# Kernel optimization log

Measured on AMD Instinct MI355X. Metric: run time of the kernel, lower is better.

Reference implementation:

```python
import jax, jax.numpy as jnp
import numpy as np

B, QLEN, MLEN, D_MODEL, N_HEAD, D_HEAD = 4, 1024, 1024, 512, 8, 64
KLEN = QLEN + MLEN


def _rel_shift(x):
    # x: [b, i, j, n] -> Transformer-XL relative shift
    b, i, j, n = x.shape
    zero_pad = jnp.zeros((b, i, 1, n), dtype=x.dtype)
    x_padded = jnp.concatenate([zero_pad, x], axis=2)          # [b, i, j+1, n]
    x_padded = x_padded.reshape(b, j + 1, i, n)
    return x_padded[:, 1:].reshape(b, i, j, n)


def setup_inputs() -> dict:
    key = jax.random.key(0)
    ks = jax.random.split(key, 9)
    x = jax.random.normal(ks[0], (B, KLEN, D_MODEL), dtype=jnp.float32)
    p = jax.random.normal(ks[1], (KLEN, D_MODEL), dtype=jnp.float32)
    w_scale = 0.02
    W_query = jax.random.normal(ks[2], (D_MODEL, N_HEAD, D_HEAD), dtype=jnp.float32) * w_scale
    W_key = jax.random.normal(ks[3], (D_MODEL, N_HEAD, D_HEAD), dtype=jnp.float32) * w_scale
    W_value = jax.random.normal(ks[4], (D_MODEL, N_HEAD, D_HEAD), dtype=jnp.float32) * w_scale
    W_out = jax.random.normal(ks[5], (D_MODEL, N_HEAD, D_HEAD), dtype=jnp.float32) * w_scale
    W_position = jax.random.normal(ks[6], (D_MODEL, N_HEAD, D_HEAD), dtype=jnp.float32) * w_scale
    bias_k = jax.random.normal(ks[7], (N_HEAD, D_HEAD), dtype=jnp.float32) * w_scale
    bias_r = jax.random.normal(ks[8], (N_HEAD, D_HEAD), dtype=jnp.float32) * w_scale
    # causal mask with memory: query i attends to keys j <= i + MLEN
    i_idx = jnp.arange(QLEN)[:, None]
    j_idx = jnp.arange(KLEN)[None, :]
    mask = j_idx > (i_idx + MLEN)  # True = masked out
    return {
        "x": x, "p": p,
        "W_query": W_query, "W_key": W_key, "W_value": W_value,
        "W_out": W_out, "W_position": W_position,
        "bias_k": bias_k, "bias_r": bias_r,
        "mask": mask, "qlen": QLEN,
    }


def reference(x, p, W_query, W_key, W_value, W_out, W_position, bias_k, bias_r, mask, qlen):
    d_head = W_query.shape[-1]
    scale = 1.0 / (d_head ** 0.5)
    q = jnp.einsum('dha,bld->blha', W_query, x[:, -qlen:])   # [b, qlen, n, d]
    k = jnp.einsum('dha,bld->blha', W_key, x)                # [b, klen, n, d]
    v = jnp.einsum('dha,bld->blha', W_value, x)              # [b, klen, n, d]
    r = jnp.einsum('dha,ld->lha', W_position, p)             # [klen, n, d]
    AC = jnp.einsum('bind,bjnd->bijn', q + bias_k, k)
    BD = jnp.einsum('bind,jnd->bijn', q + bias_r, r)
    attn_score = scale * (AC + _rel_shift(BD))               # [b, i, j, n]
    neg_inf = jnp.finfo(attn_score.dtype).min
    attn_score = jnp.where(mask[None, :, :, None], neg_inf, attn_score)
    attn_prob = jax.nn.softmax(attn_score, axis=2)
    out = jnp.einsum('bijn,bjnd->bind', attn_prob, v)        # [b, qlen, n, d]
    out = jnp.einsum('dha,blha->bld', W_out, out)            # [b, qlen, d_model]
    return out
```

## Files before the change

kernel.cpp:

```cpp
#include <hip/hip_runtime.h>
#include <hip/hip_bf16.h>
#include <stddef.h>
#include <stdint.h>

#define DM    512
#define NHEAD 8
#define DHEAD 64
#define QLEN  1024
#define KLEN  2048
#define MLEN  1024
#define B_SZ  4

typedef __attribute__((ext_vector_type(8))) short short8;
typedef __attribute__((ext_vector_type(8))) unsigned short ushort8;
typedef __attribute__((ext_vector_type(4))) float floatx4;

static __device__ __forceinline__ unsigned short f2bf(float f) {
  unsigned int u = __float_as_uint(f);
  unsigned int r = (u + 0x7FFFu + ((u >> 16) & 1u)) >> 16;
  return (unsigned short)r;
}
static __device__ __forceinline__ float bf2f(unsigned short h) {
  return __uint_as_float(((unsigned int)h) << 16);
}

template <int CTRL>
static __device__ __forceinline__ float maxdpp(float v) {
  int sh = __builtin_amdgcn_update_dpp(0, __float_as_int(v), CTRL, 0xF, 0xF, true);
  return fmaxf(v, __int_as_float(sh));
}
static __device__ __forceinline__ float rowmax16(float v) {
  v = maxdpp<0xB1>(v);
  v = maxdpp<0x4E>(v);
  v = maxdpp<0x124>(v);
  v = maxdpp<0x128>(v);
  return v;
}

#define GLOAD_LDS16(gsrc, ldst)                                               \
  __builtin_amdgcn_global_load_lds(                                           \
      (const __attribute__((address_space(1))) unsigned int*)(gsrc),          \
      (__attribute__((address_space(3))) unsigned int*)(ldst), 16, 0, 0)

__global__ __launch_bounds__(256) void k_prep(
    const float* __restrict__ x, const float* __restrict__ p,
    const float* __restrict__ Wq, const float* __restrict__ Wk,
    const float* __restrict__ Wv, const float* __restrict__ Wp,
    const float* __restrict__ Wo,
    unsigned short* __restrict__ xb, unsigned short* __restrict__ pb,
    unsigned short* __restrict__ wt,
    unsigned short* __restrict__ woh, unsigned short* __restrict__ wol) {
  __shared__ float tile[64][65];
  const int bid = blockIdx.x;
  const int tid = threadIdx.x;
  if (bid < 2048) {
    const int i = bid * 256 + tid;
    float4 a = *(const float4*)(x + (size_t)i * 8);
    float4 b = *(const float4*)(x + (size_t)i * 8 + 4);
    ushort8 o;
    o[0] = f2bf(a.x); o[1] = f2bf(a.y); o[2] = f2bf(a.z); o[3] = f2bf(a.w);
    o[4] = f2bf(b.x); o[5] = f2bf(b.y); o[6] = f2bf(b.z); o[7] = f2bf(b.w);
    *(ushort8*)(xb + (size_t)i * 8) = o;
  } else if (bid < 2560) {
    const int i = (bid - 2048) * 256 + tid;
    float4 a = *(const float4*)(p + (size_t)i * 8);
    float4 b = *(const float4*)(p + (size_t)i * 8 + 4);
    ushort8 o;
    o[0] = f2bf(a.x); o[1] = f2bf(a.y); o[2] = f2bf(a.z); o[3] = f2bf(a.w);
    o[4] = f2bf(b.x); o[5] = f2bf(b.y); o[6] = f2bf(b.z); o[7] = f2bf(b.w);
    *(ushort8*)(pb + (size_t)i * 8) = o;
  } else if (bid < 2816) {
    const int b2 = bid - 2560;
    const int nbq = b2 & 7, kbq = (b2 >> 3) & 7, z = b2 >> 6;
    const float* W = (z == 0) ? Wq : (z == 1) ? Wk : (z == 2) ? Wv : Wp;
    unsigned short* out = wt + (size_t)z * 262144;
    const int row = tid >> 2, c0 = (tid & 3) * 16;
    const int kb = kbq * 64, nb = nbq * 64;
#pragma unroll
    for (int j = 0; j < 4; ++j) {
      float4 ld = *(const float4*)(W + (size_t)(kb + row) * DM + nb + c0 + j * 4);
      tile[row][c0 + j * 4 + 0] = ld.x;
      tile[row][c0 + j * 4 + 1] = ld.y;
      tile[row][c0 + j * 4 + 2] = ld.z;
      tile[row][c0 + j * 4 + 3] = ld.w;
    }
    __syncthreads();
    unsigned short ob[16];
#pragma unroll
    for (int j = 0; j < 16; ++j) ob[j] = f2bf(tile[c0 + j][row]);
    unsigned short* orow = out + (size_t)(nb + row) * DM + kb + c0;
    *(ushort8*)(orow) = *(ushort8*)&ob[0];
    *(ushort8*)(orow + 8) = *(ushort8*)&ob[8];
  } else {
    const int i = (bid - 2816) * 256 + tid;
    ushort8 vh, vl;
#pragma unroll
    for (int j = 0; j < 8; ++j) {
      float f = Wo[(size_t)i * 8 + j];
      unsigned short h = f2bf(f);
      vh[j] = h;
      vl[j] = f2bf(f - bf2f(h));
    }
    *(ushort8*)(woh + (size_t)i * 8) = vh;
    *(ushort8*)(wol + (size_t)i * 8) = vl;
  }
}

__global__ __launch_bounds__(256) void k_vtrans(
    const unsigned short* __restrict__ v_, unsigned short* __restrict__ vt) {
  __shared__ unsigned short tile[64][72];
  const int tid = threadIdx.x;
  const int row = tid >> 2, c0 = (tid & 3) * 16;
  const int kt = blockIdx.x;
  const int bn = blockIdx.y;
  const int bb = bn >> 3, n = bn & 7;
  const unsigned short* src =
      v_ + ((size_t)(bb * KLEN) + kt * 64 + row) * DM + n * DHEAD + c0;
  *(ushort8*)&tile[row][c0] = *(const ushort8*)src;
  *(ushort8*)&tile[row][c0 + 8] = *(const ushort8*)(src + 8);
  __syncthreads();
  unsigned short ob[16];
#pragma unroll
  for (int j = 0; j < 16; ++j) ob[j] = tile[c0 + j][row];
  unsigned short* dst =
      vt + ((size_t)bn * DHEAD + row) * KLEN + kt * 64 + c0;
  *(ushort8*)dst = *(ushort8*)&ob[0];
  *(ushort8*)(dst + 8) = *(ushort8*)&ob[8];
}

__global__ __launch_bounds__(256) void k_proj_mfma(
    const unsigned short* __restrict__ xb, const unsigned short* __restrict__ pb,
    const unsigned short* __restrict__ wt,
    unsigned short* __restrict__ q_, unsigned short* __restrict__ k_,
    unsigned short* __restrict__ v_, unsigned short* __restrict__ r_) {
  __shared__ unsigned short Abuf[128 * 64];
  __shared__ unsigned short Bbuf[128 * 64];
  const int tid = threadIdx.x, w = tid >> 6, lane = tid & 63;
  const int c = lane & 15, g = lane >> 4;
  const int wr = w >> 1, wc = w & 1;
  const int mb = blockIdx.x, nb = blockIdx.y;
  int prob, mloc;
  const unsigned short* A;
  unsigned short* C;
  if (mb < 32)        { prob = 0; mloc = mb;       A = xb; C = q_; }
  else if (mb < 96)   { prob = 1; mloc = mb - 32;  A = xb; C = k_; }
  else if (mb < 160)  { prob = 2; mloc = mb - 96;  A = xb; C = v_; }
  else                { prob = 3; mloc = mb - 160; A = pb; C = r_; }
  const unsigned short* W = wt + (size_t)prob * 262144;
  const int m0 = mloc * 128;
  const int lrow = lane >> 3, lslot = lane & 7;

  floatx4 acc[4][4];
#pragma unroll
  for (int m = 0; m < 4; ++m)
#pragma unroll
    for (int nn = 0; nn < 4; ++nn) acc[m][nn] = (floatx4){0.f, 0.f, 0.f, 0.f};

  for (int k0 = 0; k0 < DM; k0 += 64) {
    __syncthreads();
#pragma unroll
    for (int iq = 0; iq < 4; ++iq) {
      const int r0 = w * 32 + iq * 8;
      const int arow = r0 + lrow;
      const int mrow = m0 + arow;
      const int grow =
          (prob == 0) ? ((mrow >> 10) * KLEN + (mrow & 1023) + MLEN) : mrow;
      const int sgA = lslot ^ (arow & 7);
      GLOAD_LDS16(A + (size_t)grow * DM + k0 + sgA * 8, Abuf + r0 * 64);
      const int nrow = nb * 128 + arow;
      GLOAD_LDS16(W + (size_t)nrow * DM + k0 + sgA * 8, Bbuf + r0 * 64);
    }
    __syncthreads();
#pragma unroll
    for (int kk = 0; kk < 2; ++kk) {
      short8 af[4], bf[4];
#pragma unroll
      for (int m = 0; m < 4; ++m) {
        const int arow = wr * 64 + m * 16 + c;
        const int slot = (kk * 4 + g) ^ (arow & 7);
        af[m] = *(const short8*)(Abuf + arow * 64 + slot * 8);
      }
#pragma unroll
      for (int nn = 0; nn < 4; ++nn) {
        const int brow = wc * 64 + nn * 16 + c;
        const int slot = (kk * 4 + g) ^ (brow & 7);
        bf[nn] = *(const short8*)(Bbuf + brow * 64 + slot * 8);
      }
#pragma unroll
      for (int m = 0; m < 4; ++m)
#pragma unroll
        for (int nn = 0; nn < 4; ++nn)
          acc[m][nn] = __builtin_amdgcn_mfma_f32_16x16x32_bf16(
              af[m], bf[nn], acc[m][nn], 0, 0, 0);
    }
  }
#pragma unroll
  for (int m = 0; m < 4; ++m)
#pragma unroll
    for (int nn = 0; nn < 4; ++nn)
#pragma unroll
      for (int rg = 0; rg < 4; ++rg) {
        const int row = m0 + wr * 64 + m * 16 + 4 * g + rg;
        const int col = nb * 128 + wc * 64 + nn * 16 + c;
        C[(size_t)row * DM + col] = f2bf(acc[m][nn][rg]);
      }
}

__global__ __launch_bounds__(256) void k_out_mfma(
    const unsigned short* __restrict__ Ah, const unsigned short* __restrict__ Al,
    const unsigned short* __restrict__ Bh, const unsigned short* __restrict__ Bl,
    float* __restrict__ C) {
  __shared__ unsigned short bufAh[64 * 64], bufAl[64 * 64];
  __shared__ unsigned short bufBh[64 * 64], bufBl[64 * 64];
  const int tid = threadIdx.x, w = tid >> 6, lane = tid & 63;
  const int c = lane & 15, g = lane >> 4;
  const int wr = w >> 1, wc = w & 1;
  const int bm = blockIdx.x, bn = blockIdx.y;
  const int lrow = lane >> 3, lslot = lane & 7;
  floatx4 acc[2][2];
#pragma unroll
  for (int mi = 0; mi < 2; ++mi)
#pragma unroll
    for (int ni = 0; ni < 2; ++ni) acc[mi][ni] = (floatx4){0.f, 0.f, 0.f, 0.f};

  for (int k0 = 0; k0 < DM; k0 += 64) {
    __syncthreads();
#pragma unroll
    for (int iq = 0; iq < 2; ++iq) {
      const int r0 = w * 16 + iq * 8;
      const int arow = r0 + lrow;
      const int sg = lslot ^ (arow & 7);
      GLOAD_LDS16(Ah + (size_t)(bm * 64 + arow) * DM + k0 + sg * 8, bufAh + r0 * 64);
      GLOAD_LDS16(Al + (size_t)(bm * 64 + arow) * DM + k0 + sg * 8, bufAl + r0 * 64);
      GLOAD_LDS16(Bh + (size_t)(bn * 64 + arow) * DM + k0 + sg * 8, bufBh + r0 * 64);
      GLOAD_LDS16(Bl + (size_t)(bn * 64 + arow) * DM + k0 + sg * 8, bufBl + r0 * 64);
    }
    __syncthreads();
#pragma unroll
    for (int kk = 0; kk < 2; ++kk) {
      short8 ah[2], al[2], bh[2], bl[2];
#pragma unroll
      for (int mi = 0; mi < 2; ++mi) {
        const int row = wr * 32 + mi * 16 + c;
        const int slot = (kk * 4 + g) ^ (row & 7);
        ah[mi] = *(const short8*)(bufAh + row * 64 + slot * 8);
        al[mi] = *(const short8*)(bufAl + row * 64 + slot * 8);
      }
#pragma unroll
      for (int ni = 0; ni < 2; ++ni) {
        const int row = wc * 32 + ni * 16 + c;
        const int slot = (kk * 4 + g) ^ (row & 7);
        bh[ni] = *(const short8*)(bufBh + row * 64 + slot * 8);
        bl[ni] = *(const short8*)(bufBl + row * 64 + slot * 8);
      }
#pragma unroll
      for (int mi = 0; mi < 2; ++mi)
#pragma unroll
        for (int ni = 0; ni < 2; ++ni) {
          acc[mi][ni] = __builtin_amdgcn_mfma_f32_16x16x32_bf16(
              ah[mi], bh[ni], acc[mi][ni], 0, 0, 0);
          acc[mi][ni] = __builtin_amdgcn_mfma_f32_16x16x32_bf16(
              al[mi], bh[ni], acc[mi][ni], 0, 0, 0);
          acc[mi][ni] = __builtin_amdgcn_mfma_f32_16x16x32_bf16(
              ah[mi], bl[ni], acc[mi][ni], 0, 0, 0);
        }
    }
  }
#pragma unroll
  for (int mi = 0; mi < 2; ++mi)
#pragma unroll
    for (int ni = 0; ni < 2; ++ni)
#pragma unroll
      for (int rg = 0; rg < 4; ++rg) {
        const int row = bm * 64 + wr * 32 + mi * 16 + 4 * g + rg;
        const int col = bn * 64 + wc * 32 + ni * 16 + c;
        C[(size_t)row * DM + col] = acc[mi][ni][rg];
      }
}

__global__ __launch_bounds__(256, 2) void k_attn_mfma(
    const unsigned short* __restrict__ q, const unsigned short* __restrict__ k,
    const unsigned short* __restrict__ vt, const unsigned short* __restrict__ r,
    const float* __restrict__ bk, const float* __restrict__ br,
    unsigned short* __restrict__ aoh, unsigned short* __restrict__ aol) {
  __shared__ unsigned short Kt[2][64 * 64];
  __shared__ unsigned short VTt[2][64 * 64];
  __shared__ unsigned short Rr[192 * 64];
  __shared__ unsigned short P[4][16][76];

  const int tid = threadIdx.x;
  const int w = tid >> 6;
  const int lane = tid & 63;
  const int c = lane & 15;
  const int g = lane >> 4;
  const int n = blockIdx.y;
  const int b = blockIdx.z;
  const int grp = (n + NHEAD * b) >> 4;
  const int i0 = (grp ? (15 - (int)blockIdx.x) : (int)blockIdx.x) * 64;
  const int qb = i0 + w * 16;

  const unsigned short* vtbn = vt + (size_t)(b * NHEAD + n) * DHEAD * KLEN;
  const unsigned short* kbase = k + (size_t)(b * KLEN) * DM + n * DHEAD;
  const unsigned short* rbase_p = r + n * DHEAD;

  const int srow = tid >> 3;
  const int sslot = tid & 7;
  const int gbase = 960 - i0;

  short8 aqk[2], aqr[2];
  {
    const unsigned short* qrow =
        q + ((size_t)(b * QLEN) + qb + c) * DM + n * DHEAD;
#pragma unroll
    for (int kb2 = 0; kb2 < 2; ++kb2) {
      short8 qv = *(const short8*)(qrow + kb2 * 32 + g * 8);
#pragma unroll
      for (int j = 0; j < 8; ++j) {
        int d = kb2 * 32 + g * 8 + j;
        float f = bf2f((unsigned short)qv[j]);
        aqk[kb2][j] = (short)f2bf((f + bk[n * DHEAD + d]) * 0.125f);
        aqr[kb2][j] = (short)f2bf((f + br[n * DHEAD + d]) * 0.125f);
      }
    }
  }

  floatx4 o[4];
#pragma unroll
  for (int t = 0; t < 4; ++t) o[t] = (floatx4){0.f, 0.f, 0.f, 0.f};
  float m[4], lsum[4], shc[4];
#pragma unroll
  for (int rg = 0; rg < 4; ++rg) { m[rg] = -1e30f; lsum[rg] = 0.f; shc[rg] = 0.f; }

  const int nkb = i0 / 64 + 17;

  auto STAGE_KV = [&](int t, int buf) {
    const int j0 = t * 64;
#pragma unroll
    for (int p = 0; p < 2; ++p) {
      const int row = p * 32 + srow;
      const int sg = sslot ^ (row & 7);
      GLOAD_LDS16(kbase + (size_t)(j0 + row) * DM + sg * 8,
                  &Kt[buf][row * 64 + sslot * 8]);
      GLOAD_LDS16(vtbn + (size_t)row * KLEN + j0 + sg * 8,
                  &VTt[buf][row * 64 + sslot * 8]);
    }
  };
  auto STAGE_R = [&](int t, int bt) {
    int sb = bt + 128; if (sb >= 192) sb -= 192;
#pragma unroll
    for (int p = 0; p < 2; ++p) {
      const int row = p * 32 + srow;
      const int slot = sb + row;
      const int grow = min(gbase + 64 * t + 128 + row, KLEN - 1);
      const int sg = sslot ^ (slot & 7);
      GLOAD_LDS16(rbase_p + (size_t)grow * DM + sg * 8,
                  &Rr[slot * 64 + sslot * 8]);
    }
  };

  STAGE_KV(0, 0);
#pragma unroll
  for (int p = 0; p < 4; ++p) {
    const int row = p * 32 + srow;
    const int grow = min(gbase + row, KLEN - 1);
    const int sg = sslot ^ (row & 7);
    GLOAD_LDS16(rbase_p + (size_t)grow * DM + sg * 8,
                &Rr[row * 64 + sslot * 8]);
  }
  __syncthreads();
  int cur = 0;
  int bt = 0;

  const int s0 = (g ^ (c & 7)) * 8;
  const int s1 = ((4 + g) ^ (c & 7)) * 8;

  for (int t = 0; t < nkb; ++t) {
    if (t + 1 < nkb) { STAGE_KV(t + 1, cur ^ 1); STAGE_R(t, bt); }
    const unsigned short* Kc = &Kt[cur][0];
    const unsigned short* Vc = &VTt[cur][0];

    float sh[5][4];
    if (t == 0) {
      const int lr = (3 - w) * 16 + c;
      const unsigned short* Rrow = Rr + lr * 64;
      short8 rf0 = *(const short8*)(Rrow + s0);
      short8 rf1 = *(const short8*)(Rrow + s1);
      floatx4 bd = (floatx4){0.f, 0.f, 0.f, 0.f};
      bd = __builtin_amdgcn_mfma_f32_16x16x32_bf16(aqr[0], rf0, bd, 0, 0, 0);
      bd = __builtin_amdgcn_mfma_f32_16x16x32_bf16(aqr[1], rf1, bd, 0, 0, 0);
#pragma unroll
      for (int rg = 0; rg < 4; ++rg) {
        const int srcl = (g << 4) | ((15 + c - 4 * g - rg) & 15);
        sh[0][rg] = __shfl(bd[rg], srcl, 64);
      }
    } else {
#pragma unroll
      for (int rg = 0; rg < 4; ++rg) sh[0][rg] = shc[rg];
    }
#pragma unroll
    for (int tau5 = 1; tau5 < 5; ++tau5) {
      const int lr = (tau5 + 3 - w) * 16 + c;
      int slot = bt + lr; if (slot >= 192) slot -= 192;
      const unsigned short* Rrow = Rr + slot * 64;
      short8 rf0 = *(const short8*)(Rrow + s0);
      short8 rf1 = *(const short8*)(Rrow + s1);
      floatx4 bd = (floatx4){0.f, 0.f, 0.f, 0.f};
      bd = __builtin_amdgcn_mfma_f32_16x16x32_bf16(aqr[0], rf0, bd, 0, 0, 0);
      bd = __builtin_amdgcn_mfma_f32_16x16x32_bf16(aqr[1], rf1, bd, 0, 0, 0);
#pragma unroll
      for (int rg = 0; rg < 4; ++rg) {
        const int srcl = (g << 4) | ((15 + c - 4 * g - rg) & 15);
        sh[tau5][rg] = __shfl(bd[rg], srcl, 64);
      }
    }
#pragma unroll
    for (int rg = 0; rg < 4; ++rg) shc[rg] = sh[4][rg];

    floatx4 s[4];
    const bool lastblk = (t == nkb - 1);
    __builtin_amdgcn_s_setprio(1);
#pragma unroll
    for (int tau = 0; tau < 4; ++tau) {
      const int kr = tau * 16 + c;
      short8 kf0 = *(const short8*)(Kc + kr * 64 + s0);
      short8 kf1 = *(const short8*)(Kc + kr * 64 + s1);
      floatx4 acc = (floatx4){0.f, 0.f, 0.f, 0.f};
      acc = __builtin_amdgcn_mfma_f32_16x16x32_bf16(aqk[0], kf0, acc, 0, 0, 0);
      acc = __builtin_amdgcn_mfma_f32_16x16x32_bf16(aqk[1], kf1, acc, 0, 0, 0);
#pragma unroll
      for (int rg = 0; rg < 4; ++rg) {
        const int ql = 4 * g + rg;
        float sv = acc[rg] + ((c > ql) ? sh[tau + 1][rg] : sh[tau][rg]);
        if (lastblk && (tau * 16 + c > w * 16 + ql)) sv = -1e30f;
        s[tau][rg] = sv;
      }
    }
    __builtin_amdgcn_s_setprio(0);

    float mx[4];
    bool ok = true;
#pragma unroll
    for (int rg = 0; rg < 4; ++rg) {
      float v2 = fmaxf(fmaxf(s[0][rg], s[1][rg]), fmaxf(s[2][rg], s[3][rg]));
      v2 = rowmax16(v2);
      mx[rg] = v2;
      ok = ok && (v2 <= m[rg] + 8.0f);
    }
    if (!__all(ok)) {
#pragma unroll
      for (int rg = 0; rg < 4; ++rg) {
        float mn = fmaxf(m[rg], mx[rg]);
        float fac = __expf(m[rg] - mn);
        m[rg] = mn;
        lsum[rg] *= fac;
#pragma unroll
        for (int td = 0; td < 4; ++td) o[td][rg] *= fac;
      }
    }
#pragma unroll
    for (int tau = 0; tau < 4; ++tau) {
#pragma unroll
      for (int rg = 0; rg < 4; ++rg) {
        float p = __expf(s[tau][rg] - m[rg]);
        lsum[rg] += p;
        P[w][4 * g + rg][tau * 16 + c] = f2bf(p);
      }
    }

    short8 pa0 = *(const short8*)&P[w][c][g * 8];
    short8 pa1 = *(const short8*)&P[w][c][32 + g * 8];
    __builtin_amdgcn_s_setprio(1);
#pragma unroll
    for (int td = 0; td < 4; ++td) {
      const int vrow = td * 16 + c;
      short8 vb0 = *(const short8*)(Vc + vrow * 64 + s0);
      short8 vb1 = *(const short8*)(Vc + vrow * 64 + s1);
      o[td] = __builtin_amdgcn_mfma_f32_16x16x32_bf16(pa0, vb0, o[td], 0, 0, 0);
      o[td] = __builtin_amdgcn_mfma_f32_16x16x32_bf16(pa1, vb1, o[td], 0, 0, 0);
    }
    __builtin_amdgcn_s_setprio(0);
    __syncthreads();
    cur ^= 1;
    bt += 64; if (bt >= 192) bt -= 192;
  }

#pragma unroll
  for (int rg = 0; rg < 4; ++rg) {
    float L = lsum[rg];
#pragma unroll
    for (int shm = 1; shm < 16; shm <<= 1) L += __shfl_xor(L, shm, 64);
    lsum[rg] = L;
  }
#pragma unroll
  for (int rg = 0; rg < 4; ++rg) {
    const int ql = 4 * g + rg;
    const float invl = 1.0f / lsum[rg];
#pragma unroll
    for (int td = 0; td < 4; ++td) {
      float val = o[td][rg] * invl;
      unsigned short hi = f2bf(val);
      float lo = val - bf2f(hi);
      size_t off = ((size_t)(b * QLEN) + qb + ql) * DM + n * DHEAD + td * 16 + c;
      aoh[off] = hi;
      aol[off] = f2bf(lo);
    }
  }
}

extern "C" void kernel_launch(void* const* d_in, const int* in_sizes, int n_in,
                              void* d_out, int out_size, void* d_ws, size_t ws_size,
                              hipStream_t stream) {
  const float* x  = (const float*)d_in[0];
  const float* p  = (const float*)d_in[1];
  const float* Wq = (const float*)d_in[2];
  const float* Wk = (const float*)d_in[3];
  const float* Wv = (const float*)d_in[4];
  const float* Wo = (const float*)d_in[5];
  const float* Wp = (const float*)d_in[6];
  const float* bk = (const float*)d_in[7];
  const float* br = (const float*)d_in[8];
  float* out = (float*)d_out;

  unsigned short* q_  = (unsigned short*)d_ws;
  unsigned short* k_  = q_  + (size_t)2097152;
  unsigned short* v_  = k_  + (size_t)4194304;
  unsigned short* r_  = v_  + (size_t)4194304;
  unsigned short* xb  = r_  + (size_t)1048576;
  unsigned short* pb  = xb  + (size_t)4194304;
  unsigned short* wt  = pb  + (size_t)1048576;
  unsigned short* woh = wt  + (size_t)1048576;
  unsigned short* wol = woh + (size_t)262144;
  unsigned short* aoh = wol + (size_t)262144;
  unsigned short* aol = aoh + (size_t)2097152;
  unsigned short* vt_ = aol + (size_t)2097152;

  k_prep<<<2944, 256, 0, stream>>>(x, p, Wq, Wk, Wv, Wp, Wo,
                                   xb, pb, wt, woh, wol);
  k_proj_mfma<<<dim3(176, 4), 256, 0, stream>>>(xb, pb, wt, q_, k_, v_, r_);
  k_vtrans<<<dim3(KLEN / 64, NHEAD * B_SZ), 256, 0, stream>>>(v_, vt_);
  k_attn_mfma<<<dim3(16, 8, 4), 256, 0, stream>>>(
      q_, k_, vt_, r_, bk, br, aoh, aol);
  k_out_mfma<<<dim3(64, 8), 256, 0, stream>>>(aoh, aol, woh, wol, out);
}
```

Before: 115.6 us.

## Split attention key range across two wave groups with LDS merge

The attention kernel now launches 512 threads per block. Two groups of four waves each process half of the key range, using 32-wide key tiles instead of 64-wide. Group 1 writes its partial output, max and sum to shared memory, and group 0 merges them with a flash-decoding-style rescale before the final store. The aim is to double the waves per block, hide latency better, and shorten the per-block serial loop. In exchange it adds a combine step, an extra barrier and larger shared memory use, which may limit occupancy.

```diff
diff --git a/kernel.cpp b/kernel.cpp
--- a/kernel.cpp
+++ b/kernel.cpp
@@ -278,18 +278,23 @@
       }
 }
 
-__global__ __launch_bounds__(256, 2) void k_attn_mfma(
+__global__ __launch_bounds__(512, 4) void k_attn_mfma(
     const unsigned short* __restrict__ q, const unsigned short* __restrict__ k,
     const unsigned short* __restrict__ vt, const unsigned short* __restrict__ r,
     const float* __restrict__ bk, const float* __restrict__ br,
     unsigned short* __restrict__ aoh, unsigned short* __restrict__ aol) {
-  __shared__ unsigned short Kt[2][64 * 64];
-  __shared__ unsigned short VTt[2][64 * 64];
-  __shared__ unsigned short Rr[192 * 64];
-  __shared__ unsigned short P[4][16][76];
+  __shared__ alignas(16) char SMEM[75776];
+  unsigned short* Kt  = (unsigned short*)SMEM;
+  unsigned short* VTt = (unsigned short*)(SMEM + 16384);
+  unsigned short* Rr  = (unsigned short*)(SMEM + 32768);
+  unsigned short* P   = (unsigned short*)(SMEM + 65536);
+  float* oC  = (float*)SMEM;
+  float* mlC = (float*)(SMEM + 17408);
 
   const int tid = threadIdx.x;
-  const int w = tid >> 6;
+  const int wave = tid >> 6;
+  const int h = wave >> 2;
+  const int w = wave & 3;
   const int lane = tid & 63;
   const int c = lane & 15;
   const int g = lane >> 4;
@@ -303,9 +308,9 @@
   const unsigned short* kbase = k + (size_t)(b * KLEN) * DM + n * DHEAD;
   const unsigned short* rbase_p = r + n * DHEAD;
 
-  const int srow = tid >> 3;
-  const int sslot = tid & 7;
-  const int gbase = 960 - i0;
+  const int nkb = i0 / 32 + 34;
+  const int nIt = nkb >> 1;
+  const int g0r = 960 - i0;
 
   short8 aqk[2], aqr[2];
   {
@@ -331,157 +336,174 @@
 #pragma unroll
   for (int rg = 0; rg < 4; ++rg) { m[rg] = -1e30f; lsum[rg] = 0.f; shc[rg] = 0.f; }
 
-  const int nkb = i0 / 64 + 17;
-
-  auto STAGE_KV = [&](int t, int buf) {
-    const int j0 = t * 64;
-#pragma unroll
-    for (int p = 0; p < 2; ++p) {
-      const int row = p * 32 + srow;
-      const int sg = sslot ^ (row & 7);
-      GLOAD_LDS16(kbase + (size_t)(j0 + row) * DM + sg * 8,
-                  &Kt[buf][row * 64 + sslot * 8]);
-      GLOAD_LDS16(vtbn + (size_t)row * KLEN + j0 + sg * 8,
-                  &VTt[buf][row * 64 + sslot * 8]);
+  int bt = 0;
+
+  auto STAGE = [&](int itn) {
+    const int buf = itn & 1;
+    const int hh = tid >> 8;
+    const int idx = tid & 255;
+    const int tn = hh * nIt + itn;
+    {
+      const int row = idx >> 3, slot = idx & 7;
+      GLOAD_LDS16(kbase + (size_t)(32 * tn + row) * DM + (slot ^ (row & 7)) * 8,
+                  Kt + (hh * 2 + buf) * 2048 + idx * 8);
+    }
+    {
+      const int row = idx >> 2, slot = idx & 3;
+      GLOAD_LDS16(vtbn + (size_t)row * KLEN + 32 * tn +
+                      ((slot ^ ((row >> 1) & 3)) * 8),
+                  VTt + (hh * 2 + buf) * 2048 + idx * 8);
+    }
+    {
+      const int row = idx >> 3, slot = idx & 7;
+      const int sb = (bt + 96) & 127;
+      const int gst = g0r + hh * (32 * nIt);
+      const int grow = min(gst + 32 * itn + 64 + row, KLEN - 1);
+      GLOAD_LDS16(rbase_p + (size_t)grow * DM + (slot ^ (row & 7)) * 8,
+                  Rr + hh * 8192 + (sb + row) * 64 + slot * 8);
     }
   };
-  auto STAGE_R = [&](int t, int bt) {
-    int sb = bt + 128; if (sb >= 192) sb -= 192;
-#pragma unroll
-    for (int p = 0; p < 2; ++p) {
-      const int row = p * 32 + srow;
-      const int slot = sb + row;
-      const int grow = min(gbase + 64 * t + 128 + row, KLEN - 1);
-      const int sg = sslot ^ (slot & 7);
-      GLOAD_LDS16(rbase_p + (size_t)grow * DM + sg * 8,
-                  &Rr[slot * 64 + sslot * 8]);
-    }
-  };
-
-  STAGE_KV(0, 0);
-#pragma unroll
-  for (int p = 0; p < 4; ++p) {
-    const int row = p * 32 + srow;
-    const int grow = min(gbase + row, KLEN - 1);
-    const int sg = sslot ^ (row & 7);
-    GLOAD_LDS16(rbase_p + (size_t)grow * DM + sg * 8,
-                &Rr[row * 64 + sslot * 8]);
+
+  {
+    const int hh = tid >> 8;
+    const int idx = tid & 255;
+    const int tn = hh * nIt;
+    {
+      const int row = idx >> 3, slot = idx & 7;
+      GLOAD_LDS16(kbase + (size_t)(32 * tn + row) * DM + (slot ^ (row & 7)) * 8,
+                  Kt + (hh * 2) * 2048 + idx * 8);
+    }
+    {
+      const int row = idx >> 2, slot = idx & 3;
+      GLOAD_LDS16(vtbn + (size_t)row * KLEN + 32 * tn +
+                      ((slot ^ ((row >> 1) & 3)) * 8),
+                  VTt + (hh * 2) * 2048 + idx * 8);
+    }
+  }
+#pragma unroll
+  for (int p = 0; p < 3; ++p) {
+    const int Lr = tid + p * 512;
+    const int hh = (Lr >= 768) ? 1 : 0;
+    const int idx = Lr - hh * 768;
+    const int row = idx >> 3, slot = idx & 7;
+    const int gst = g0r + hh * (32 * nIt);
+    const int grow = min(gst + row, KLEN - 1);
+    GLOAD_LDS16(rbase_p + (size_t)grow * DM + (slot ^ (row & 7)) * 8,
+                Rr + hh * 8192 + row * 64 + slot * 8);
   }
   __syncthreads();
-  int cur = 0;
-  int bt = 0;
 
   const int s0 = (g ^ (c & 7)) * 8;
   const int s1 = ((4 + g) ^ (c & 7)) * 8;
-
-  for (int t = 0; t < nkb; ++t) {
-    if (t + 1 < nkb) { STAGE_KV(t + 1, cur ^ 1); STAGE_R(t, bt); }
-    const unsigned short* Kc = &Kt[cur][0];
-    const unsigned short* Vc = &VTt[cur][0];
-
-    float sh[5][4];
-    if (t == 0) {
-      const int lr = (3 - w) * 16 + c;
-      const unsigned short* Rrow = Rr + lr * 64;
-      short8 rf0 = *(const short8*)(Rrow + s0);
-      short8 rf1 = *(const short8*)(Rrow + s1);
-      floatx4 bd = (floatx4){0.f, 0.f, 0.f, 0.f};
-      bd = __builtin_amdgcn_mfma_f32_16x16x32_bf16(aqr[0], rf0, bd, 0, 0, 0);
-      bd = __builtin_amdgcn_mfma_f32_16x16x32_bf16(aqr[1], rf1, bd, 0, 0, 0);
+  const int vs0 = (g ^ ((c >> 1) & 3)) * 8;
+  unsigned short* Pw = P + (size_t)wave * 640;
+
+  for (int it = 0; it < nIt; ++it) {
+    if (it + 1 < nIt) STAGE(it + 1);
+    const int t = h * nIt + it;
+    const bool act = (32 * t <= qb + 15 + MLEN);
+    if (act) {
+      const unsigned short* Kc = Kt + (h * 2 + (it & 1)) * 2048;
+      const unsigned short* Vc = VTt + (h * 2 + (it & 1)) * 2048;
+      const unsigned short* Rh = Rr + h * 8192;
+
+      float sh[3][4];
+      if (it == 0) {
+        const int rs = ((bt + 16 * (3 - w)) & 127) + c;
+        const unsigned short* Rrow = Rh + rs * 64;
+        short8 rf0 = *(const short8*)(Rrow + s0);
+        short8 rf1 = *(const short8*)(Rrow + s1);
+        floatx4 bd = (floatx4){0.f, 0.f, 0.f, 0.f};
+        bd = __builtin_amdgcn_mfma_f32_16x16x32_bf16(aqr[0], rf0, bd, 0, 0, 0);
+        bd = __builtin_amdgcn_mfma_f32_16x16x32_bf16(aqr[1], rf1, bd, 0, 0, 0);
+#pragma unroll
+        for (int rg = 0; rg < 4; ++rg) {
+          const int srcl = (g << 4) | ((15 + c - 4 * g - rg) & 15);
+          sh[0][rg] = __shfl(bd[rg], srcl, 64);
+        }
+      } else {
+#pragma unroll
+        for (int rg = 0; rg < 4; ++rg) sh[0][rg] = shc[rg];
+      }
+#pragma unroll
+      for (int t5 = 1; t5 < 3; ++t5) {
+        const int rs = ((bt + 16 * (t5 + 3 - w)) & 127) + c;
+        const unsigned short* Rrow = Rh + rs * 64;
+        short8 rf0 = *(const short8*)(Rrow + s0);
+        short8 rf1 = *(const short8*)(Rrow + s1);
+        floatx4 bd = (floatx4){0.f, 0.f, 0.f, 0.f};
+        bd = __builtin_amdgcn_mfma_f32_16x16x32_bf16(aqr[0], rf0, bd, 0, 0, 0);
+        bd = __builtin_amdgcn_mfma_f32_16x16x32_bf16(aqr[1], rf1, bd, 0, 0, 0);
+#pragma unroll
+        for (int rg = 0; rg < 4; ++rg) {
+          const int srcl = (g << 4) | ((15 + c - 4 * g - rg) & 15);
+          sh[t5][rg] = __shfl(bd[rg], srcl, 64);
+        }
+      }
+#pragma unroll
+      for (int rg = 0; rg < 4; ++rg) shc[rg] = sh[2][rg];
+
+      const int thr = qb + MLEN - 32 * t;
+      floatx4 s[2];
+      __builtin_amdgcn_s_setprio(1);
+#pragma unroll
+      for (int tau = 0; tau < 2; ++tau) {
+        const int kr = tau * 16 + c;
+        short8 kf0 = *(const short8*)(Kc + kr * 64 + s0);
+        short8 kf1 = *(const short8*)(Kc + kr * 64 + s1);
+        floatx4 acc = (floatx4){0.f, 0.f, 0.f, 0.f};
+        acc = __builtin_amdgcn_mfma_f32_16x16x32_bf16(aqk[0], kf0, acc, 0, 0, 0);
+        acc = __builtin_amdgcn_mfma_f32_16x16x32_bf16(aqk[1], kf1, acc, 0, 0, 0);
+#pragma unroll
+        for (int rg = 0; rg < 4; ++rg) {
+          const int ql = 4 * g + rg;
+          float sv = acc[rg] + ((c > ql) ? sh[tau + 1][rg] : sh[tau][rg]);
+          if (tau * 16 + c > thr + ql) sv = -1e30f;
+          s[tau][rg] = sv;
+        }
+      }
+      __builtin_amdgcn_s_setprio(0);
+
+      float mx[4];
+      bool ok = true;
 #pragma unroll
       for (int rg = 0; rg < 4; ++rg) {
-        const int srcl = (g << 4) | ((15 + c - 4 * g - rg) & 15);
-        sh[0][rg] = __shfl(bd[rg], srcl, 64);
-      }
-    } else {
-#pragma unroll
-      for (int rg = 0; rg < 4; ++rg) sh[0][rg] = shc[rg];
-    }
-#pragma unroll
-    for (int tau5 = 1; tau5 < 5; ++tau5) {
-      const int lr = (tau5 + 3 - w) * 16 + c;
-      int slot = bt + lr; if (slot >= 192) slot -= 192;
-      const unsigned short* Rrow = Rr + slot * 64;
-      short8 rf0 = *(const short8*)(Rrow + s0);
-      short8 rf1 = *(const short8*)(Rrow + s1);
-      floatx4 bd = (floatx4){0.f, 0.f, 0.f, 0.f};
-      bd = __builtin_amdgcn_mfma_f32_16x16x32_bf16(aqr[0], rf0, bd, 0, 0, 0);
-      bd = __builtin_amdgcn_mfma_f32_16x16x32_bf16(aqr[1], rf1, bd, 0, 0, 0);
-#pragma unroll
-      for (int rg = 0; rg < 4; ++rg) {
-        const int srcl = (g << 4) | ((15 + c - 4 * g - rg) & 15);
-        sh[tau5][rg] = __shfl(bd[rg], srcl, 64);
-      }
-    }
-#pragma unroll
-    for (int rg = 0; rg < 4; ++rg) shc[rg] = sh[4][rg];
-
-    floatx4 s[4];
-    const bool lastblk = (t == nkb - 1);
-    __builtin_amdgcn_s_setprio(1);
-#pragma unroll
-    for (int tau = 0; tau < 4; ++tau) {
-      const int kr = tau * 16 + c;
-      short8 kf0 = *(const short8*)(Kc + kr * 64 + s0);
-      short8 kf1 = *(const short8*)(Kc + kr * 64 + s1);
-      floatx4 acc = (floatx4){0.f, 0.f, 0.f, 0.f};
-      acc = __builtin_amdgcn_mfma_f32_16x16x32_bf16(aqk[0], kf0, acc, 0, 0, 0);
-      acc = __builtin_amdgcn_mfma_f32_16x16x32_bf16(aqk[1], kf1, acc, 0, 0, 0);
-#pragma unroll
-      for (int rg = 0; rg < 4; ++rg) {
-        const int ql = 4 * g + rg;
-        float sv = acc[rg] + ((c > ql) ? sh[tau + 1][rg] : sh[tau][rg]);
-        if (lastblk && (tau * 16 + c > w * 16 + ql)) sv = -1e30f;
-        s[tau][rg] = sv;
-      }
-    }
-    __builtin_amdgcn_s_setprio(0);
-
-    float mx[4];
-    bool ok = true;
-#pragma unroll
-    for (int rg = 0; rg < 4; ++rg) {
-      float v2 = fmaxf(fmaxf(s[0][rg], s[1][rg]), fmaxf(s[2][rg], s[3][rg]));
-      v2 = rowmax16(v2);
-      mx[rg] = v2;
-      ok = ok && (v2 <= m[rg] + 8.0f);
-    }
-    if (!__all(ok)) {
-#pragma unroll
-      for (int rg = 0; rg < 4; ++rg) {
-        float mn = fmaxf(m[rg], mx[rg]);
-        float fac = __expf(m[rg] - mn);
-        m[rg] = mn;
-        lsum[rg] *= fac;
-#pragma unroll
-        for (int td = 0; td < 4; ++td) o[td][rg] *= fac;
-      }
-    }
-#pragma unroll
-    for (int tau = 0; tau < 4; ++tau) {
-#pragma unroll
-      for (int rg = 0; rg < 4; ++rg) {
-        float p = __expf(s[tau][rg] - m[rg]);
-        lsum[rg] += p;
-        P[w][4 * g + rg][tau * 16 + c] = f2bf(p);
-      }
-    }
-
-    short8 pa0 = *(const short8*)&P[w][c][g * 8];
-    short8 pa1 = *(const short8*)&P[w][c][32 + g * 8];
-    __builtin_amdgcn_s_setprio(1);
-#pragma unroll
-    for (int td = 0; td < 4; ++td) {
-      const int vrow = td * 16 + c;
-      short8 vb0 = *(const short8*)(Vc + vrow * 64 + s0);
-      short8 vb1 = *(const short8*)(Vc + vrow * 64 + s1);
-      o[td] = __builtin_amdgcn_mfma_f32_16x16x32_bf16(pa0, vb0, o[td], 0, 0, 0);
-      o[td] = __builtin_amdgcn_mfma_f32_16x16x32_bf16(pa1, vb1, o[td], 0, 0, 0);
-    }
-    __builtin_amdgcn_s_setprio(0);
+        float v2 = rowmax16(fmaxf(s[0][rg], s[1][rg]));
+        mx[rg] = v2;
+        ok = ok && (v2 <= m[rg] + 8.0f);
+      }
+      if (!__all(ok)) {
+#pragma unroll
+        for (int rg = 0; rg < 4; ++rg) {
+          float mn = fmaxf(m[rg], mx[rg]);
+          float fac = __expf(m[rg] - mn);
+          m[rg] = mn;
+          lsum[rg] *= fac;
+#pragma unroll
+          for (int td = 0; td < 4; ++td) o[td][rg] *= fac;
+        }
+      }
+#pragma unroll
+      for (int tau = 0; tau < 2; ++tau) {
+#pragma unroll
+        for (int rg = 0; rg < 4; ++rg) {
+          float p = __expf(s[tau][rg] - m[rg]);
+          lsum[rg] += p;
+          Pw[(4 * g + rg) * 40 + tau * 16 + c] = f2bf(p);
+        }
+      }
+
+      short8 pa = *(const short8*)(Pw + c * 40 + g * 8);
+      __builtin_amdgcn_s_setprio(1);
+#pragma unroll
+      for (int td = 0; td < 4; ++td) {
+        short8 vb = *(const short8*)(Vc + (td * 16 + c) * 32 + vs0);
+        o[td] = __builtin_amdgcn_mfma_f32_16x16x32_bf16(pa, vb, o[td], 0, 0, 0);
+      }
+      __builtin_amdgcn_s_setprio(0);
+    }
     __syncthreads();
-    cur ^= 1;
-    bt += 64; if (bt >= 192) bt -= 192;
+    bt = (bt + 32) & 127;
   }
 
 #pragma unroll
@@ -491,18 +513,40 @@
     for (int shm = 1; shm < 16; shm <<= 1) L += __shfl_xor(L, shm, 64);
     lsum[rg] = L;
   }
-#pragma unroll
-  for (int rg = 0; rg < 4; ++rg) {
-    const int ql = 4 * g + rg;
-    const float invl = 1.0f / lsum[rg];
-#pragma unroll
-    for (int td = 0; td < 4; ++td) {
-      float val = o[td][rg] * invl;
-      unsigned short hi = f2bf(val);
-      float lo = val - bf2f(hi);
-      size_t off = ((size_t)(b * QLEN) + qb + ql) * DM + n * DHEAD + td * 16 + c;
-      aoh[off] = hi;
-      aol[off] = f2bf(lo);
+
+  if (h == 1) {
+#pragma unroll
+    for (int rg = 0; rg < 4; ++rg) {
+      const int ql = 4 * g + rg;
+#pragma unroll
+      for (int td = 0; td < 4; ++td)
+        oC[(w * 16 + ql) * 68 + td * 16 + c] = o[td][rg];
+      if (c == 0) {
+        mlC[w * 32 + ql] = m[rg];
+        mlC[w * 32 + 16 + ql] = lsum[rg];
+      }
+    }
+  }
+  __syncthreads();
+  if (h == 0) {
+#pragma unroll
+    for (int rg = 0; rg < 4; ++rg) {
+      const int ql = 4 * g + rg;
+      const float m1 = mlC[w * 32 + ql];
+      const float l1 = mlC[w * 32 + 16 + ql];
+      const float M = fmaxf(m[rg], m1);
+      const float w0 = __expf(m[rg] - M);
+      const float w1 = __expf(m1 - M);
+      const float invl = 1.0f / (lsum[rg] * w0 + l1 * w1);
+#pragma unroll
+      for (int td = 0; td < 4; ++td) {
+        float val = (o[td][rg] * w0 + oC[(w * 16 + ql) * 68 + td * 16 + c] * w1) * invl;
+        unsigned short hi = f2bf(val);
+        float lo = val - bf2f(hi);
+        size_t off = ((size_t)(b * QLEN) + qb + ql) * DM + n * DHEAD + td * 16 + c;
+        aoh[off] = hi;
+        aol[off] = f2bf(lo);
+      }
     }
   }
 }
@@ -538,7 +582,7 @@
                                    xb, pb, wt, woh, wol);
   k_proj_mfma<<<dim3(176, 4), 256, 0, stream>>>(xb, pb, wt, q_, k_, v_, r_);
   k_vtrans<<<dim3(KLEN / 64, NHEAD * B_SZ), 256, 0, stream>>>(v_, vt_);
-  k_attn_mfma<<<dim3(16, 8, 4), 256, 0, stream>>>(
+  k_attn_mfma<<<dim3(16, 8, 4), 512, 0, stream>>>(
       q_, k_, vt_, r_, bk, br, aoh, aol);
   k_out_mfma<<<dim3(64, 8), 256, 0, stream>>>(aoh, aol, woh, wol, out);
 }
```

After: 111.5 us. 1.04x faster.
